# Kernel tuning notes

Measured on AMD Instinct MI355X. Metric: run time of the kernel, lower is better.

Reference implementation:

```python
import jax, jax.numpy as jnp
import numpy as np


def _unfold2d(x, side):
    # x: (B, C, H, W) -> (B, C, out, out, side, side), stride-1 sliding windows
    H = x.shape[2]
    out = H - side + 1
    idx = jnp.arange(out)[:, None] + jnp.arange(side)[None, :]  # (out, side)
    x = x[:, :, idx, :]        # (B, C, out, side, W)
    x = x[:, :, :, :, idx]     # (B, C, out, side, out, side)
    return jnp.transpose(x, (0, 1, 2, 4, 3, 5))  # (B, C, out, out, side, side)


def setup_inputs() -> dict:
    key = jax.random.key(0)
    k1, k2, k3 = jax.random.split(key, 3)
    img, side, num = 128, 5, 25
    out = img - side + 1  # 124
    x = jax.random.normal(k1, (1, 3, img, img), dtype=jnp.float32)
    w = jax.random.normal(k2, (3, out, out, num, side, side), dtype=jnp.float32)
    q = jax.random.normal(k3, (3, out, out, num, side, side), dtype=jnp.float32)
    return {"x": x, "w": w, "q": q}


def reference(x, w, q):
    side = w.shape[-1]
    # patches: (1, 3, out, out, 1, side, side) -- broadcast replaces torch repeat
    p = _unfold2d(x, side)[:, :, :, :, None, :, :]
    y = (jnp.pi + 2.0 * jnp.arctan(10.0 * (p * w - q))) / (2.0 * jnp.pi)
    y = jnp.log(jnp.prod(y + 0.6, axis=6))  # product over last window dim, then log
    y = jnp.sum(y, axis=5)                   # sum over remaining window dim
    return y  # (1, 3, out, out, num)
```

## Files before the change

kernel.cpp:

```cpp
#include <hip/hip_runtime.h>


#define IMG   128
#define OUT   124
#define NUM   25
#define SIDE  5
#define NOUT  (3 * OUT * OUT * NUM)
#define WTOT  ((long long)NOUT * NUM)
#define OPB   256
#define FPB   (OPB * NUM)
#define FPB4  (FPB / 4)

__device__ __forceinline__ float fast_atan(float z) {
    float az  = __builtin_fabsf(z);
    float r   = __builtin_amdgcn_rcpf(az);
    bool  big = az > 1.0f;
    float t   = big ? r : az;
    float s   = t * t;
    float p   =                     -0.01172120f;
    p = __builtin_fmaf(p, s,         0.05265332f);
    p = __builtin_fmaf(p, s,        -0.11643287f);
    p = __builtin_fmaf(p, s,         0.19354346f);
    p = __builtin_fmaf(p, s,        -0.33262347f);
    p = __builtin_fmaf(p, s,         0.99997726f);
    float a = t * p;
    a = big ? (1.57079632679489662f - a) : a;
    return __builtin_copysignf(a, z);
}

__global__ __launch_bounds__(OPB) void dendrite_kernel(
    const float* __restrict__ x,
    const float* __restrict__ w,
    const float* __restrict__ q,
    float* __restrict__ out)
{
    __shared__ float lw[FPB];
    __shared__ float lq[FPB];

    const int t   = threadIdx.x;
    const int blk = blockIdx.x;
    const long long base = (long long)blk * FPB;

    const float4* w4 = (const float4*)(w + base);
    const float4* q4 = (const float4*)(q + base);
    float4* lw4 = (float4*)lw;
    float4* lq4 = (float4*)lq;
    const int nf4 = (int)(((WTOT - base) < (long long)FPB ? (WTOT - base) : (long long)FPB) >> 2);
    #pragma unroll
    for (int idx = t; idx < FPB4; idx += OPB) {
        if (idx < nf4) {
            lw4[idx] = w4[idx];
            lq4[idx] = q4[idx];
        }
    }
    __syncthreads();

    const int o = blk * OPB + t;
    if (o < NOUT) {
        int rem = o / NUM;
        const int j = rem % OUT;  rem /= OUT;
        const int i = rem % OUT;
        const int c = rem / OUT;

        const float* xp = x + ((long long)c * IMG + i) * IMG + j;
        const float* wp = lw + t * NUM;
        const float* qp = lq + t * NUM;

        float acc = 0.0f;
        #pragma unroll
        for (int u = 0; u < SIDE; ++u) {
            float prod = 1.0f;
            #pragma unroll
            for (int v = 0; v < SIDE; ++v) {
                const float pv = xp[u * IMG + v];
                const int   k  = u * SIDE + v;
                const float z  = 10.0f * __builtin_fmaf(pv, wp[k], -qp[k]);
                const float a  = fast_atan(z);
                prod *= __builtin_fmaf(a, 0.31830988618379067f, 1.1f);
            }
            acc += __logf(prod);
        }
        out[o] = acc;
    }
}

extern "C" void kernel_launch(void* const* d_in, const int* in_sizes, int n_in,
                              void* d_out, int out_size, void* d_ws, size_t ws_size,
                              hipStream_t stream) {
    const float* x = (const float*)d_in[0];
    const float* w = (const float*)d_in[1];
    const float* q = (const float*)d_in[2];
    float* out = (float*)d_out;

    const int grid = (NOUT + OPB - 1) / OPB;
    dendrite_kernel<<<grid, OPB, 0, stream>>>(x, w, q, out);
}
```

Baseline: 248.5 us.

## Load weights directly into registers and fold per-row logs into one log

Measured after the change: 246.5 us. No clear change (-0.8%).

```diff
diff --git a/kernel.cpp b/kernel.cpp
--- a/kernel.cpp
+++ b/kernel.cpp
@@ -4,12 +4,8 @@
 #define IMG   128
 #define OUT   124
 #define NUM   25
-#define SIDE  5
 #define NOUT  (3 * OUT * OUT * NUM)
-#define WTOT  ((long long)NOUT * NUM)
 #define OPB   256
-#define FPB   (OPB * NUM)
-#define FPB4  (FPB / 4)
 
 __device__ __forceinline__ float fast_atan(float z) {
     float az  = __builtin_fabsf(z);
@@ -28,60 +24,59 @@
     return __builtin_copysignf(a, z);
 }
 
+__device__ __forceinline__ float4 load4u(const float* p) {
+    float4 v;
+    __builtin_memcpy(&v, p, sizeof(float4));
+    return v;
+}
+
 __global__ __launch_bounds__(OPB) void dendrite_kernel(
     const float* __restrict__ x,
     const float* __restrict__ w,
     const float* __restrict__ q,
     float* __restrict__ out)
 {
-    __shared__ float lw[FPB];
-    __shared__ float lq[FPB];
+    const int o = blockIdx.x * OPB + threadIdx.x;
+    if (o >= NOUT) return;
 
-    const int t   = threadIdx.x;
-    const int blk = blockIdx.x;
-    const long long base = (long long)blk * FPB;
+    int rem = o / NUM;
+    const int j = rem % OUT;  rem /= OUT;
+    const int i = rem % OUT;
+    const int c = rem / OUT;
 
-    const float4* w4 = (const float4*)(w + base);
-    const float4* q4 = (const float4*)(q + base);
-    float4* lw4 = (float4*)lw;
-    float4* lq4 = (float4*)lq;
-    const int nf4 = (int)(((WTOT - base) < (long long)FPB ? (WTOT - base) : (long long)FPB) >> 2);
+    const float* wp = w + (long long)o * NUM;
+    const float* qp = q + (long long)o * NUM;
+    const float* xp = x + ((long long)c * IMG + i) * IMG + j;
+
+    float wv[NUM], qv[NUM], xv[NUM];
     #pragma unroll
-    for (int idx = t; idx < FPB4; idx += OPB) {
-        if (idx < nf4) {
-            lw4[idx] = w4[idx];
-            lq4[idx] = q4[idx];
-        }
+    for (int g = 0; g < 6; ++g) {
+        float4 a = load4u(wp + 4 * g);
+        wv[4*g+0] = a.x; wv[4*g+1] = a.y; wv[4*g+2] = a.z; wv[4*g+3] = a.w;
     }
-    __syncthreads();
+    wv[24] = wp[24];
+    #pragma unroll
+    for (int g = 0; g < 6; ++g) {
+        float4 a = load4u(qp + 4 * g);
+        qv[4*g+0] = a.x; qv[4*g+1] = a.y; qv[4*g+2] = a.z; qv[4*g+3] = a.w;
+    }
+    qv[24] = qp[24];
+    #pragma unroll
+    for (int u = 0; u < 5; ++u) {
+        float4 a = load4u(xp + u * IMG);
+        xv[5*u+0] = a.x; xv[5*u+1] = a.y; xv[5*u+2] = a.z; xv[5*u+3] = a.w;
+        xv[5*u+4] = xp[u * IMG + 4];
+    }
 
-    const int o = blk * OPB + t;
-    if (o < NOUT) {
-        int rem = o / NUM;
-        const int j = rem % OUT;  rem /= OUT;
-        const int i = rem % OUT;
-        const int c = rem / OUT;
-
-        const float* xp = x + ((long long)c * IMG + i) * IMG + j;
-        const float* wp = lw + t * NUM;
-        const float* qp = lq + t * NUM;
-
-        float acc = 0.0f;
-        #pragma unroll
-        for (int u = 0; u < SIDE; ++u) {
-            float prod = 1.0f;
-            #pragma unroll
-            for (int v = 0; v < SIDE; ++v) {
-                const float pv = xp[u * IMG + v];
-                const int   k  = u * SIDE + v;
-                const float z  = 10.0f * __builtin_fmaf(pv, wp[k], -qp[k]);
-                const float a  = fast_atan(z);
-                prod *= __builtin_fmaf(a, 0.31830988618379067f, 1.1f);
-            }
-            acc += __logf(prod);
-        }
-        out[o] = acc;
+    float prod0 = 1.0f, prod1 = 1.0f;
+    #pragma unroll
+    for (int k = 0; k < NUM; ++k) {
+        const float z = 10.0f * __builtin_fmaf(xv[k], wv[k], -qv[k]);
+        const float a = fast_atan(z);
+        const float term = __builtin_fmaf(a, 0.31830988618379067f, 1.1f);
+        if (k & 1) prod1 *= term; else prod0 *= term;
     }
+    out[o] = __logf(prod0 * prod1);
 }
 
 extern "C" void kernel_launch(void* const* d_in, const int* in_sizes, int n_in,
```
